# Kernel optimization log

Measured on AMD Instinct MI355X. Metric: run time of the kernel, lower is better.

## Reference

```python
import jax, jax.numpy as jnp
import numpy as np

B, S, D = 4, 2048, 1024
MAG_SCALE = 5.0


def setup_inputs() -> dict:
    key = jax.random.key(0)
    ks = jax.random.split(key, 16)
    sd = 1.0 / np.sqrt(D)  # keep pre-activations O(1)
    inp = {
        "x": jax.random.normal(ks[0], (B, S, D), jnp.float32),
        "W_omega": jax.random.normal(ks[1], (D, D), jnp.float32) * sd,
        "b_omega": jnp.zeros((D,), jnp.float32),
        "W_mag": jax.random.normal(ks[2], (D, D), jnp.float32) * sd,
        "b_mag": jnp.zeros((D,), jnp.float32),
        "W_phi0": jax.random.normal(ks[3], (D, D), jnp.float32) * sd,
        "b_phi0": jnp.zeros((D,), jnp.float32),
        "W_gate": jax.random.normal(ks[4], (D, D), jnp.float32) * sd,
        "b_gate": jnp.zeros((D,), jnp.float32),
        "W_q": jax.random.normal(ks[5], (D, D), jnp.float32) * sd,
        "b_q": jnp.zeros((D,), jnp.float32),
        "integration_scale": jax.random.uniform(ks[6], (D,), jnp.float32),
        "W_out": jax.random.normal(ks[7], (4 * D, D), jnp.float32) * (1.0 / np.sqrt(4 * D)),
        "b_out": jnp.zeros((D,), jnp.float32),
    }
    return inp


def reference(x, W_omega, b_omega, W_mag, b_mag, W_phi0, b_phi0,
              W_gate, b_gate, W_q, b_q, integration_scale, W_out, b_out):
    lin = lambda h, W, b: h @ W + b  # [B,S,*] @ [*,Dout]

    omega = lin(x, W_omega, b_omega)                      # phase velocity [B,S,D]
    magnitude = jax.nn.sigmoid(lin(x, W_mag, b_mag)) * MAG_SCALE
    gate = jax.nn.sigmoid(lin(x, W_gate, b_gate))
    gated_omega = gate * (omega * jnp.abs(integration_scale))
    phi = lin(x, W_phi0, b_phi0) + jnp.cumsum(gated_omega, axis=1)  # integrated phase

    cos_phi = jnp.cos(phi)
    sin_phi = jnp.sin(phi)

    # holographic memory write: cumulative complex binding of content with phase
    weighted_content = magnitude * x
    memory_real = jnp.cumsum(weighted_content * cos_phi, axis=1)
    memory_imag = jnp.cumsum(weighted_content * sin_phi, axis=1)
    sqrt_mag = jnp.sqrt(jnp.cumsum(magnitude, axis=1) + 1e-8)
    memory_real = memory_real / sqrt_mag
    memory_imag = memory_imag / sqrt_mag

    # complex retrieval at a query phase
    phi_q = phi + lin(x, W_q, b_q)
    cos_q, sin_q = jnp.cos(phi_q), jnp.sin(phi_q)
    retrieved_real = memory_real * cos_q + memory_imag * sin_q
    retrieved_imag = memory_imag * cos_q - memory_real * sin_q

    context = jnp.concatenate(
        [x * cos_phi, x * sin_phi, retrieved_real, retrieved_imag], axis=-1)  # [B,S,4D]
    return x + lin(context, W_out, b_out)


if __name__ == "__main__":
    out = reference(**setup_inputs())
    print(out.shape, out.dtype)
```

## Files before the change

### kernel.cpp

```cpp
#include <hip/hip_runtime.h>
#include <hip/hip_fp16.h>

#define B_ 4
#define S_ 2048
#define D_ 1024
#define CCH 128
#define LCH 16
#define NELEM ((size_t)B_*S_*D_)
#define MROWS (B_*S_)

typedef __attribute__((ext_vector_type(4))) float f32x4;
typedef __attribute__((ext_vector_type(8))) _Float16 f16x8;

__device__ __forceinline__ ushort f2h(float v) {
  __half h = __float2half(v);
  return __builtin_bit_cast(ushort, h);
}
__device__ __forceinline__ float h2f(ushort u) {
  return __half2float(__builtin_bit_cast(__half, u));
}

__device__ __forceinline__ void gload16(const ushort* src, char* ldsdst) {
  __builtin_amdgcn_global_load_lds(
      (const __attribute__((address_space(1))) void*)src,
      (__attribute__((address_space(3))) void*)ldsdst, 16, 0, 0);
}


__global__ void xhalf_kernel(const float* __restrict__ x, ushort* __restrict__ xh) {
  size_t i = ((size_t)blockIdx.x * blockDim.x + threadIdx.x) * 8;
  if (i >= NELEM) return;
  float4 a = *(const float4*)(x + i);
  float4 b = *(const float4*)(x + i + 4);
  ushort h[8] = {f2h(a.x), f2h(a.y), f2h(a.z), f2h(a.w),
                 f2h(b.x), f2h(b.y), f2h(b.z), f2h(b.w)};
  *(ushort4*)(xh + i) = *(ushort4*)h;
  *(ushort4*)(xh + i + 4) = *(ushort4*)(h + 4);
}

__global__ void transpose5(const float* __restrict__ W0, const float* __restrict__ W1,
                           const float* __restrict__ W2, const float* __restrict__ W3,
                           const float* __restrict__ W4, ushort* __restrict__ Th) {
  __shared__ float tile[64][65];
  const int z = blockIdx.z;
  const float* W = (z == 0) ? W0 : (z == 1) ? W1 : (z == 2) ? W2 : (z == 3) ? W3 : W4;
  ushort* T = Th + (size_t)z * D_ * D_;
  const int k0 = blockIdx.x * 64, n0 = blockIdx.y * 64;
  const int tx = threadIdx.x & 63, ty = threadIdx.x >> 6;
#pragma unroll
  for (int i = 0; i < 16; ++i)
    tile[ty * 16 + i][tx] = W[(size_t)(k0 + ty * 16 + i) * D_ + n0 + tx];
  __syncthreads();
#pragma unroll
  for (int i = 0; i < 16; ++i) {
    const int nn = ty * 16 + i;
    T[(size_t)(n0 + nn) * D_ + k0 + tx] = f2h(tile[tx][nn]);
  }
}

__global__ void transpose_convert(const float* __restrict__ W, ushort* __restrict__ Th, int sh,
                                  int Kd, int Nd) {
  __shared__ float tile[64][65];
  const int k0 = blockIdx.x * 64, n0 = blockIdx.y * 64;
  const int tx = threadIdx.x & 63, ty = threadIdx.x >> 6;
#pragma unroll
  for (int i = 0; i < 16; ++i)
    tile[ty * 16 + i][tx] = W[(size_t)(k0 + ty * 16 + i) * Nd + n0 + tx];
  __syncthreads();
#pragma unroll
  for (int i = 0; i < 16; ++i) {
    const int nn = ty * 16 + i;
    Th[(size_t)(n0 + nn) * sh + k0 + tx] = f2h(tile[tx][nn]);
  }
}

template <int FINAL, int BN>
__global__ __launch_bounds__(512, 2) void gemmT(
    const ushort* __restrict__ A, int lda, const ushort* __restrict__ Bw,
    ushort* __restrict__ Ch, ushort* __restrict__ C4h,
    float* __restrict__ Cf, const float* __restrict__ xres, const float* __restrict__ bias,
    int M, int K) {
  constexpr int SLICE = 8192 + BN * 64;
  constexpr int JJ = BN / 64;
  __shared__ __align__(16) char ldsc[3 * SLICE];
  const int bid = blockIdx.x;
  const int tm = bid & 63, tn = bid >> 6;
  const int ldb = K;
  const int NT = K >> 5;
  const int t = threadIdx.x, lane = t & 63, wid = t >> 6;
  const int wm = wid >> 2, wn = wid & 3;

  f32x4 acc[4][JJ];
#pragma unroll
  for (int i = 0; i < 4; ++i)
#pragma unroll
    for (int j = 0; j < JJ; ++j) acc[i][j] = (f32x4){0.f, 0.f, 0.f, 0.f};

  const int line1 = t >> 3;
  const int g8s = (t & 7) ^ (line1 & 7);
  const int rowS = line1 * 2 + (g8s >> 2);
  const int kgS = (g8s & 3) << 3;
  const ushort* srcA = A + (size_t)(tm * 128 + rowS) * lda + kgS;
  const ushort* srcB = Bw + (size_t)(tn * BN + rowS) * ldb + kgS;
  char* dstA = ldsc + (size_t)t * 16;
  char* dstB = ldsc + 8192 + (size_t)t * 16;

  auto STAGE = [&](int tile, int slot) {
    const int ts = (tile < NT) ? tile : NT - 1;
    char* ba = dstA + slot * SLICE;
    char* bb = dstB + slot * SLICE;
    gload16(srcA + ts * 32, ba);
    gload16(srcB + ts * 32, bb);
    if (BN == 256) gload16(srcB + (size_t)128 * ldb + ts * 32, bb + 8192);
  };
#define WAIT_OLDEST()                                               \
  if (BN == 256) { asm volatile("s_waitcnt vmcnt(3)" ::: "memory"); } \
  else           { asm volatile("s_waitcnt vmcnt(2)" ::: "memory"); }

  const int lane15 = lane & 15;
  const int hl = lane15 >> 1;
  const int swz = ((((lane15 & 1) << 2) + (lane >> 4)) ^ hl) << 4;
  const char* aB = ldsc + wm * 4096 + hl * 128 + swz;
  const char* bB = ldsc + 8192 + wn * ((BN / 4) * 64) + hl * 128 + swz;

  STAGE(0, 0); STAGE(1, 1);
  WAIT_OLDEST();
  __builtin_amdgcn_sched_barrier(0);
  __builtin_amdgcn_s_barrier();

  int s_rd = 0, s_st = 2;
#pragma unroll 1
  for (int tt = 0; tt < NT; ++tt) {
    STAGE(tt + 2, s_st);
    const char* ab = aB + s_rd * SLICE;
    const char* bb = bB + s_rd * SLICE;
    f16x8 af[4], bf_[JJ];
#pragma unroll
    for (int f = 0; f < 4; ++f) af[f] = *(const f16x8*)(ab + f * 1024);
#pragma unroll
    for (int c = 0; c < JJ; ++c) bf_[c] = *(const f16x8*)(bb + c * 1024);
    asm volatile("s_waitcnt lgkmcnt(0)" ::: "memory");
    __builtin_amdgcn_sched_barrier(0);
    __builtin_amdgcn_s_setprio(1);
#pragma unroll
    for (int f = 0; f < 4; ++f)
#pragma unroll
      for (int c = 0; c < JJ; ++c)
        acc[f][c] = __builtin_amdgcn_mfma_f32_16x16x32_f16(af[f], bf_[c], acc[f][c], 0, 0, 0);
    __builtin_amdgcn_s_setprio(0);
    WAIT_OLDEST();
    __builtin_amdgcn_sched_barrier(0);
    __builtin_amdgcn_s_barrier();
    s_rd = (s_rd == 2) ? 0 : s_rd + 1;
    s_st = (s_st == 2) ? 0 : s_st + 1;
  }
#undef WAIT_OLDEST

#pragma unroll
  for (int i = 0; i < 4; ++i) {
    const int row0 = tm * 128 + wm * 64 + i * 16 + ((lane >> 4) << 2);
#pragma unroll
    for (int jj = 0; jj < JJ; ++jj) {
      const int col = tn * BN + wn * (BN / 4) + jj * 16 + lane15;
      if (FINAL) {
#pragma unroll
        for (int r = 0; r < 4; ++r) {
          const size_t idx = (size_t)(row0 + r) * 1024 + col;
          Cf[idx] = acc[i][jj][r] + xres[idx] + bias[col];
        }
      } else {
        const int pl = col >> 10;
        ushort* base = (pl < 4) ? (Ch + (size_t)pl * (size_t)M * 1024) : C4h;
#pragma unroll
        for (int r = 0; r < 4; ++r)
          base[(size_t)(row0 + r) * 1024 + (col & 1023)] = f2h(acc[i][jj][r]);
      }
    }
  }
}


__device__ __forceinline__ void load4h(const ushort* p, float* f) {
  ushort4 u = *(const ushort4*)p;
  f[0] = h2f(u.x); f[1] = h2f(u.y); f[2] = h2f(u.z); f[3] = h2f(u.w);
}

__global__ void prep_chunk_kernel(ushort* __restrict__ omega_go, const ushort* __restrict__ gate_lin,
                                  ushort* __restrict__ mag_io,
                                  const float* __restrict__ b_om, const float* __restrict__ b_gate,
                                  const float* __restrict__ b_mag, const float* __restrict__ isc,
                                  float* __restrict__ gsum, float* __restrict__ msum) {
  int tid = blockIdx.x * blockDim.x + threadIdx.x;
  if (tid >= B_ * CCH * (D_ / 4)) return;
  int d4 = tid & 255, c = (tid >> 8) & (CCH - 1), b = tid >> 15;
  int d = d4 * 4;
  size_t base = ((size_t)(b * S_) + c * LCH) * D_ + d;
  size_t cs = ((size_t)(b * CCH) + c) * D_ + d;
  float bo[4], bg[4], bm[4], is[4];
  *(float4*)bo = *(const float4*)(b_om + d);
  *(float4*)bg = *(const float4*)(b_gate + d);
  *(float4*)bm = *(const float4*)(b_mag + d);
  *(float4*)is = *(const float4*)(isc + d);
  float sg[4] = {0.f, 0.f, 0.f, 0.f}, sm[4] = {0.f, 0.f, 0.f, 0.f};
  for (int s = 0; s < LCH; ++s) {
    size_t i = base + (size_t)s * D_;
    float om[4], gl[4], mg[4];
    load4h(omega_go + i, om);
    load4h(gate_lin + i, gl);
    load4h(mag_io + i, mg);
    ushort wo[4], wm_[4];
#pragma unroll
    for (int j = 0; j < 4; ++j) {
      float g = 1.f / (1.f + __expf(-(gl[j] + bg[j])));
      float m5 = 5.f / (1.f + __expf(-(mg[j] + bm[j])));
      float go = g * ((om[j] + bo[j]) * fabsf(is[j]));
      sg[j] += go;
      sm[j] += m5;
      wo[j] = f2h(go);
      wm_[j] = f2h(m5);
    }
    *(ushort4*)(omega_go + i) = *(ushort4*)wo;
    *(ushort4*)(mag_io + i) = *(ushort4*)wm_;
  }
  *(float4*)(gsum + cs) = *(float4*)sg;
  *(float4*)(msum + cs) = *(float4*)sm;
}

__global__ void scan_offsets_kernel(float* __restrict__ s1, float* __restrict__ s2) {
  int gw = (blockIdx.x * blockDim.x + threadIdx.x) >> 6;
  int lane = threadIdx.x & 63;
  if (gw >= B_ * D_) return;
  int d = gw & (D_ - 1), b = gw >> 10;
  float c1 = 0.f, c2 = 0.f;
#pragma unroll
  for (int h = 0; h < 2; ++h) {
    size_t idx = ((size_t)(b * CCH) + h * 64 + lane) * D_ + d;
    float v1 = s1[idx], v2 = s2[idx];
#pragma unroll
    for (int off = 1; off < 64; off <<= 1) {
      float u1 = __shfl_up(v1, off);
      float u2 = __shfl_up(v2, off);
      if (lane >= off) { v1 += u1; v2 += u2; }
    }
    float e1 = __shfl_up(v1, 1), e2 = __shfl_up(v2, 1);
    if (lane == 0) { e1 = 0.f; e2 = 0.f; }
    s1[idx] = e1 + c1;
    s2[idx] = e2 + c2;
    c1 += __shfl(v1, 63);
    c2 += __shfl(v2, 63);
  }
}

__global__ void phase_scan_kernel(const ushort* __restrict__ xh, const ushort* __restrict__ go,
                                  const ushort* __restrict__ mag, const ushort* __restrict__ p0,
                                  const float* __restrict__ goff,
                                  float* __restrict__ trsum, float* __restrict__ tisum,
                                  const float* __restrict__ b_phi, ushort* __restrict__ ctx) {
  int tid = blockIdx.x * blockDim.x + threadIdx.x;
  if (tid >= B_ * CCH * (D_ / 4)) return;
  int d4 = tid & 255, c = (tid >> 8) & (CCH - 1), b = tid >> 15;
  int d = d4 * 4;
  size_t base = ((size_t)(b * S_) + c * LCH) * D_ + d;
  size_t cs = ((size_t)(b * CCH) + c) * D_ + d;
  float pr[4], bp[4];
  *(float4*)pr = *(const float4*)(goff + cs);
  *(float4*)bp = *(const float4*)(b_phi + d);
  float tr[4] = {0.f, 0.f, 0.f, 0.f}, ti[4] = {0.f, 0.f, 0.f, 0.f};
  size_t crow = ((size_t)(b * S_ + c * LCH)) * 4096 + d;
  for (int s = 0; s < LCH; ++s) {
    size_t i = base + (size_t)s * D_;
    float g[4], ph0[4], m[4], xv[4];
    load4h(go + i, g);
    load4h(p0 + i, ph0);
    load4h(mag + i, m);
    load4h(xh + i, xv);
    ushort c4[4], s4[4];
#pragma unroll
    for (int j = 0; j < 4; ++j) {
      pr[j] += g[j];
      float ph = ph0[j] + bp[j] + pr[j];
      float sp, cp;
      __sincosf(ph, &sp, &cp);
      float wr = m[j] * xv[j];
      tr[j] += wr * cp;
      ti[j] += wr * sp;
      c4[j] = f2h(xv[j] * cp);
      s4[j] = f2h(xv[j] * sp);
    }
    *(ushort4*)(ctx + crow) = *(ushort4*)c4;
    *(ushort4*)(ctx + crow + 1024) = *(ushort4*)s4;
    crow += 4096;
  }
  *(float4*)(trsum + cs) = *(float4*)tr;
  *(float4*)(tisum + cs) = *(float4*)ti;
}

__global__ void retrieve_kernel(const ushort* __restrict__ xh, const ushort* __restrict__ go,
                                const ushort* __restrict__ mag, const ushort* __restrict__ p0,
                                const ushort* __restrict__ q,
                                const float* __restrict__ goff, const float* __restrict__ moff,
                                const float* __restrict__ troff, const float* __restrict__ tioff,
                                const float* __restrict__ b_phi, const float* __restrict__ b_q,
                                ushort* __restrict__ ctx) {
  int tid = blockIdx.x * blockDim.x + threadIdx.x;
  if (tid >= B_ * CCH * (D_ / 4)) return;
  int d4 = tid & 255, c = (tid >> 8) & (CCH - 1), b = tid >> 15;
  int d = d4 * 4;
  size_t base = ((size_t)(b * S_) + c * LCH) * D_ + d;
  size_t cs = ((size_t)(b * CCH) + c) * D_ + d;
  float pr[4], mr[4], tr[4], ti[4], bp[4], bq[4];
  *(float4*)pr = *(const float4*)(goff + cs);
  *(float4*)mr = *(const float4*)(moff + cs);
  *(float4*)tr = *(const float4*)(troff + cs);
  *(float4*)ti = *(const float4*)(tioff + cs);
  *(float4*)bp = *(const float4*)(b_phi + d);
  *(float4*)bq = *(const float4*)(b_q + d);
  size_t crow = ((size_t)(b * S_ + c * LCH)) * 4096 + d;
  for (int s = 0; s < LCH; ++s) {
    size_t i = base + (size_t)s * D_;
    float g[4], ph0[4], m[4], xv[4], qv[4];
    load4h(go + i, g);
    load4h(p0 + i, ph0);
    load4h(mag + i, m);
    load4h(q + i, qv);
    load4h(xh + i, xv);
    ushort r2[4], r3[4];
#pragma unroll
    for (int j = 0; j < 4; ++j) {
      pr[j] += g[j];
      float ph = ph0[j] + bp[j] + pr[j];
      float sp, cp;
      __sincosf(ph, &sp, &cp);
      mr[j] += m[j];
      float wr = m[j] * xv[j];
      tr[j] += wr * cp;
      ti[j] += wr * sp;
      float rs = rsqrtf(mr[j] + 1e-8f);
      float mreal = tr[j] * rs, mimag = ti[j] * rs;
      float phq = ph + qv[j] + bq[j];
      float sq, cq;
      __sincosf(phq, &sq, &cq);
      r2[j] = f2h(mreal * cq + mimag * sq);
      r3[j] = f2h(mimag * cq - mreal * sq);
    }
    *(ushort4*)(ctx + crow + 2048) = *(ushort4*)r2;
    *(ushort4*)(ctx + crow + 3072) = *(ushort4*)r3;
    crow += 4096;
  }
}

extern "C" void kernel_launch(void* const* d_in, const int* in_sizes, int n_in,
                              void* d_out, int out_size, void* d_ws, size_t ws_size,
                              hipStream_t stream) {
  const float* x      = (const float*)d_in[0];
  const float* W_om   = (const float*)d_in[1];
  const float* b_om   = (const float*)d_in[2];
  const float* W_mag  = (const float*)d_in[3];
  const float* b_mag  = (const float*)d_in[4];
  const float* W_phi  = (const float*)d_in[5];
  const float* b_phi  = (const float*)d_in[6];
  const float* W_gate = (const float*)d_in[7];
  const float* b_gate = (const float*)d_in[8];
  const float* W_q    = (const float*)d_in[9];
  const float* b_q    = (const float*)d_in[10];
  const float* isc    = (const float*)d_in[11];
  const float* W_out  = (const float*)d_in[12];
  const float* b_out  = (const float*)d_in[13];
  float* out = (float*)d_out;

  const size_t WS_NEEDED = 213909504ull;
  if (ws_size < WS_NEEDED) {
    (void)hipMemsetAsync(d_out, 0, (size_t)out_size * sizeof(float), stream);
    return;
  }
  char* w = (char*)d_ws;
  ushort* planes_h = (ushort*)w;
  ushort* omega_buf = planes_h;
  ushort* gate_buf  = planes_h + NELEM;
  ushort* mag_buf   = planes_h + 2 * NELEM;
  ushort* phi0_buf  = planes_h + 3 * NELEM;
  ushort* x_h   = (ushort*)(w + 67108864);
  ushort* q_buf = (ushort*)out;
  float* gsum  = (float*)(w + 83886080);
  float* msum  = (float*)(w + 85983232);
  float* trsum = (float*)(w + 88080384);
  float* tisum = (float*)(w + 90177536);
  char* ctxb = w + 4 * NELEM * 4;
  ushort* ctx   = (ushort*)ctxb;
  ushort* W5T   = (ushort*)(ctxb + 16777216);
  ushort* WoutT = (ushort*)(w + 201326592);

  xhalf_kernel<<<(int)(NELEM / 2048), 256, 0, stream>>>(x, x_h);
  transpose5<<<dim3(16, 16, 5), 256, 0, stream>>>(W_om, W_gate, W_mag, W_phi, W_q, W5T);
  transpose_convert<<<dim3(64, 16), 256, 0, stream>>>(W_out, WoutT, 4096, 4 * D_, D_);

  gemmT<0, 256><<<1280, 512, 0, stream>>>(x_h, 1024, W5T, planes_h, q_buf,
                                          nullptr, nullptr, nullptr, MROWS, 1024);

  prep_chunk_kernel<<<B_ * CCH * (D_ / 4) / 256, 256, 0, stream>>>(
      omega_buf, gate_buf, mag_buf, b_om, b_gate, b_mag, isc, gsum, msum);
  scan_offsets_kernel<<<B_ * D_ * 64 / 256, 256, 0, stream>>>(gsum, msum);
  phase_scan_kernel<<<B_ * CCH * (D_ / 4) / 256, 256, 0, stream>>>(
      x_h, omega_buf, mag_buf, phi0_buf, gsum, trsum, tisum, b_phi, ctx);
  scan_offsets_kernel<<<B_ * D_ * 64 / 256, 256, 0, stream>>>(trsum, tisum);
  retrieve_kernel<<<B_ * CCH * (D_ / 4) / 256, 256, 0, stream>>>(
      x_h, omega_buf, mag_buf, phi0_buf, q_buf, gsum, msum, trsum, tisum, b_phi, b_q, ctx);

  gemmT<1, 256><<<256, 512, 0, stream>>>(ctx, 4096, WoutT, nullptr, nullptr, out,
                                         x, b_out, MROWS, 4 * D_);
}
```

Baseline: 288.6 us.

## Load GEMM A operand directly into registers, stage only B through LDS

The GEMM kernel now reads A fragments straight from global memory into registers each k-step instead of staging them through LDS, so only B tiles go through the triple-buffered shared-memory pipeline. LDS use and the wait logic shrink, and launch bounds are raised to allow four blocks per CU. The final output GEMM also switches to BN=128 with twice the blocks for better CU coverage. The trade-off is uncoalesced, un-prefetched global loads for A on the critical path, which depend on cache hits to hide latency.

```diff
diff --git a/kernel.cpp b/kernel.cpp
--- a/kernel.cpp
+++ b/kernel.cpp
@@ -75,12 +75,12 @@
 }
 
 template <int FINAL, int BN>
-__global__ __launch_bounds__(512, 2) void gemmT(
+__global__ __launch_bounds__(512, 4) void gemmA(
     const ushort* __restrict__ A, int lda, const ushort* __restrict__ Bw,
     ushort* __restrict__ Ch, ushort* __restrict__ C4h,
     float* __restrict__ Cf, const float* __restrict__ xres, const float* __restrict__ bias,
     int M, int K) {
-  constexpr int SLICE = 8192 + BN * 64;
+  constexpr int SLICE = BN * 64;
   constexpr int JJ = BN / 64;
   __shared__ __align__(16) char ldsc[3 * SLICE];
   const int bid = blockIdx.x;
@@ -100,61 +100,61 @@
   const int g8s = (t & 7) ^ (line1 & 7);
   const int rowS = line1 * 2 + (g8s >> 2);
   const int kgS = (g8s & 3) << 3;
-  const ushort* srcA = A + (size_t)(tm * 128 + rowS) * lda + kgS;
   const ushort* srcB = Bw + (size_t)(tn * BN + rowS) * ldb + kgS;
-  char* dstA = ldsc + (size_t)t * 16;
-  char* dstB = ldsc + 8192 + (size_t)t * 16;
+  char* dstB = ldsc + (size_t)t * 16;
 
   auto STAGE = [&](int tile, int slot) {
     const int ts = (tile < NT) ? tile : NT - 1;
-    char* ba = dstA + slot * SLICE;
     char* bb = dstB + slot * SLICE;
-    gload16(srcA + ts * 32, ba);
     gload16(srcB + ts * 32, bb);
     if (BN == 256) gload16(srcB + (size_t)128 * ldb + ts * 32, bb + 8192);
   };
-#define WAIT_OLDEST()                                               \
-  if (BN == 256) { asm volatile("s_waitcnt vmcnt(3)" ::: "memory"); } \
-  else           { asm volatile("s_waitcnt vmcnt(2)" ::: "memory"); }
+#define WAIT_PRE()                                                              \
+  if (BN == 256) { asm volatile("s_waitcnt vmcnt(2) lgkmcnt(0)" ::: "memory"); } \
+  else           { asm volatile("s_waitcnt vmcnt(1) lgkmcnt(0)" ::: "memory"); }
 
   const int lane15 = lane & 15;
+  const ushort* srcA = A + (size_t)(tm * 128 + wm * 64 + lane15) * lda + ((lane >> 4) << 3);
+
   const int hl = lane15 >> 1;
   const int swz = ((((lane15 & 1) << 2) + (lane >> 4)) ^ hl) << 4;
-  const char* aB = ldsc + wm * 4096 + hl * 128 + swz;
-  const char* bB = ldsc + 8192 + wn * ((BN / 4) * 64) + hl * 128 + swz;
+  const char* bB = ldsc + wn * ((BN / 4) * 64) + hl * 128 + swz;
 
   STAGE(0, 0); STAGE(1, 1);
-  WAIT_OLDEST();
+  if (BN == 256) { asm volatile("s_waitcnt vmcnt(2)" ::: "memory"); }
+  else           { asm volatile("s_waitcnt vmcnt(1)" ::: "memory"); }
   __builtin_amdgcn_sched_barrier(0);
   __builtin_amdgcn_s_barrier();
 
   int s_rd = 0, s_st = 2;
 #pragma unroll 1
   for (int tt = 0; tt < NT; ++tt) {
+    f16x8 afR[4];
+    const ushort* pa = srcA + tt * 32;
+#pragma unroll
+    for (int f = 0; f < 4; ++f) afR[f] = *(const f16x8*)(pa + (size_t)(f * 16) * lda);
+    __builtin_amdgcn_sched_barrier(0);
     STAGE(tt + 2, s_st);
-    const char* ab = aB + s_rd * SLICE;
+    __builtin_amdgcn_sched_barrier(0);
     const char* bb = bB + s_rd * SLICE;
-    f16x8 af[4], bf_[JJ];
-#pragma unroll
-    for (int f = 0; f < 4; ++f) af[f] = *(const f16x8*)(ab + f * 1024);
+    f16x8 bf_[JJ];
 #pragma unroll
     for (int c = 0; c < JJ; ++c) bf_[c] = *(const f16x8*)(bb + c * 1024);
-    asm volatile("s_waitcnt lgkmcnt(0)" ::: "memory");
+    WAIT_PRE();
     __builtin_amdgcn_sched_barrier(0);
     __builtin_amdgcn_s_setprio(1);
 #pragma unroll
     for (int f = 0; f < 4; ++f)
 #pragma unroll
       for (int c = 0; c < JJ; ++c)
-        acc[f][c] = __builtin_amdgcn_mfma_f32_16x16x32_f16(af[f], bf_[c], acc[f][c], 0, 0, 0);
+        acc[f][c] = __builtin_amdgcn_mfma_f32_16x16x32_f16(afR[f], bf_[c], acc[f][c], 0, 0, 0);
     __builtin_amdgcn_s_setprio(0);
-    WAIT_OLDEST();
     __builtin_amdgcn_sched_barrier(0);
     __builtin_amdgcn_s_barrier();
     s_rd = (s_rd == 2) ? 0 : s_rd + 1;
     s_st = (s_st == 2) ? 0 : s_st + 1;
   }
-#undef WAIT_OLDEST
+#undef WAIT_PRE
 
 #pragma unroll
   for (int i = 0; i < 4; ++i) {
@@ -394,7 +394,7 @@
   transpose5<<<dim3(16, 16, 5), 256, 0, stream>>>(W_om, W_gate, W_mag, W_phi, W_q, W5T);
   transpose_convert<<<dim3(64, 16), 256, 0, stream>>>(W_out, WoutT, 4096, 4 * D_, D_);
 
-  gemmT<0, 256><<<1280, 512, 0, stream>>>(x_h, 1024, W5T, planes_h, q_buf,
+  gemmA<0, 256><<<1280, 512, 0, stream>>>(x_h, 1024, W5T, planes_h, q_buf,
                                           nullptr, nullptr, nullptr, MROWS, 1024);
 
   prep_chunk_kernel<<<B_ * CCH * (D_ / 4) / 256, 256, 0, stream>>>(
@@ -406,6 +406,6 @@
   retrieve_kernel<<<B_ * CCH * (D_ / 4) / 256, 256, 0, stream>>>(
       x_h, omega_buf, mag_buf, phi0_buf, q_buf, gsum, msum, trsum, tisum, b_phi, b_q, ctx);
 
-  gemmT<1, 256><<<256, 512, 0, stream>>>(ctx, 4096, WoutT, nullptr, nullptr, out,
+  gemmA<1, 128><<<512, 512, 0, stream>>>(ctx, 4096, WoutT, nullptr, nullptr, out,
                                          x, b_out, MROWS, 4 * D_);
 }
```

After: 570.5 us. 1.98x slower.
